# Kernel optimization log

Measured on AMD Instinct MI355X. Metric: run time of the kernel, lower is better.

Reference implementation:

```python
import jax, jax.numpy as jnp
import numpy as np

N = 50000      # num nodes
E = 1_600_000  # num edges
D = 64         # in_dim == hidden_dim
H = 4          # heads
C = 16         # head_dim = hidden_dim // heads
NEG = 0.2      # leaky_relu negative slope (PyG GATConv default)


def setup_inputs() -> dict:
    key = jax.random.key(0)
    ks = jax.random.split(key, 20)
    f = lambda k, s: (jax.random.normal(k, s, jnp.float32) * 0.1)
    return dict(
        node_features=jax.random.normal(ks[0], (N, D), jnp.float32),
        edge_index=jax.random.randint(ks[1], (2, E), 0, N, dtype=jnp.int32),
        edge_type=jax.random.randint(ks[2], (E,), 0, 5, dtype=jnp.int32),
        edge_attr=jax.random.normal(ks[3], (E, 1), jnp.float32),
        # GAT layer 1 (PyG GATConv: lin has no bias, att_* are [H,C], final bias [H*C])
        W1=f(ks[4], (D, H * C)), att_src1=f(ks[5], (H, C)), att_dst1=f(ks[6], (H, C)),
        We1=f(ks[7], (1, H * C)), att_e1=f(ks[8], (H, C)), b1=jnp.zeros((H * C,), jnp.float32),
        # GAT layer 2
        W2=f(ks[9], (D, H * C)), att_src2=f(ks[10], (H, C)), att_dst2=f(ks[11], (H, C)),
        We2=f(ks[12], (1, H * C)), att_e2=f(ks[13], (H, C)), b2=jnp.zeros((H * C,), jnp.float32),
        # LayerNorms
        g1=jnp.ones((D,), jnp.float32), beta1=jnp.zeros((D,), jnp.float32),
        g2=jnp.ones((D,), jnp.float32), beta2=jnp.zeros((D,), jnp.float32),
        # output head
        Wout=f(ks[14], (D, 1)), bout=jnp.zeros((1,), jnp.float32),
    )


def _layernorm(x, g, b, eps=1e-5):
    mu = x.mean(-1, keepdims=True)
    v = ((x - mu) ** 2).mean(-1, keepdims=True)
    return (x - mu) * jax.lax.rsqrt(v + eps) * g + b


def _seg_softmax(alpha, dst, n):
    # numerically stable segment softmax over incoming edges of each dst node
    m = jax.ops.segment_max(alpha, dst, num_segments=n)
    m = jnp.where(jnp.isfinite(m), m, 0.0)
    ex = jnp.exp(alpha - m[dst])
    den = jax.ops.segment_sum(ex, dst, num_segments=n)
    return ex / (den[dst] + 1e-16)


def _gatconv(x, src, dst, eattr, W, a_s, a_d, We, a_e, b, n):
    xs = (x @ W).reshape(n, H, C)                       # [N,H,C]
    a_src = jnp.einsum('nhc,hc->nh', xs, a_s)           # [N,H]
    a_dst = jnp.einsum('nhc,hc->nh', xs, a_d)           # [N,H]
    ee = (eattr @ We).reshape(-1, H, C)                 # [E',H,C]
    a_edge = jnp.einsum('ehc,hc->eh', ee, a_e)          # [E',H]
    alpha = a_src[src] + a_dst[dst] + a_edge            # [E',H]
    alpha = jax.nn.leaky_relu(alpha, NEG)
    alpha = _seg_softmax(alpha, dst, n)                 # [E',H]
    msg = xs[src] * alpha[..., None]                    # [E',H,C] gather-weighted messages
    out = jax.ops.segment_sum(msg, dst, num_segments=n) # scatter-aggregate
    return out.reshape(n, H * C) + b


def reference(node_features, edge_index, edge_type, edge_attr,
              W1, att_src1, att_dst1, We1, att_e1, b1,
              W2, att_src2, att_dst2, We2, att_e2, b2,
              g1, beta1, g2, beta2, Wout, bout):
    src, dst = edge_index[0], edge_index[1]
    # PyG add_self_loops(fill_value='mean'): self-loop edge_attr = mean of edge_attr over incoming edges
    cnt = jax.ops.segment_sum(jnp.ones((E,), jnp.float32), dst, num_segments=N)
    loop_attr = jax.ops.segment_sum(edge_attr, dst, num_segments=N) / jnp.maximum(cnt, 1.0)[:, None]
    loops = jnp.arange(N, dtype=src.dtype)
    src2 = jnp.concatenate([src, loops])
    dst2 = jnp.concatenate([dst, loops])
    ea = jnp.concatenate([edge_attr, loop_attr], axis=0)

    residual = node_features  # in_dim == hidden_dim -> no res_proj
    h = _gatconv(node_features, src2, dst2, ea, W1, att_src1, att_dst1, We1, att_e1, b1, N)
    h = jax.nn.elu(_layernorm(h + residual, g1, beta1))
    residual = h
    h = _gatconv(h, src2, dst2, ea, W2, att_src2, att_dst2, We2, att_e2, b2, N)
    h = jax.nn.elu(_layernorm(h + residual, g2, beta2))
    return h @ Wout + bout
```

## Files before the change

### kernel.cpp

```cpp
#include <hip/hip_runtime.h>
#include <hip/hip_bf16.h>
#include <cfloat>

#define NN 50000
#define NE 1600000
#define NEG 0.2f
#define NBKT 782
#define BNODE 64
#define P1_TILE 2048
#define P1_BLOCKS 782
#define BCAP 2560
#define SLOTS 96
#define L2E 1.4426950408889634f

typedef __attribute__((ext_vector_type(8))) short bf8_t;
typedef __attribute__((ext_vector_type(4))) float f4_t;

__device__ __forceinline__ float bf16bits_to_f(unsigned v) {
  return __uint_as_float(v << 16);
}
__device__ __forceinline__ unsigned f_to_bf16bits(float f) {
  unsigned u = __float_as_uint(f);
  return (u + 0x7fffu + ((u >> 16) & 1u)) >> 16;
}

__global__ __launch_bounds__(256) void bin_kernel(
    const int* __restrict__ src, const int* __restrict__ dst,
    const float* __restrict__ ea, int* __restrict__ gcnt,
    int2* __restrict__ gbuf) {
  __shared__ int lcnt[NBKT];
  __shared__ int lcur[NBKT];
  int t = threadIdx.x;
  for (int i = t; i < NBKT; i += 256) lcnt[i] = 0;
  __syncthreads();
  int e0 = blockIdx.x * P1_TILE;
  int bb[8], vx[8], vy[8];
#pragma unroll
  for (int k = 0; k < 8; ++k) {
    int e = e0 + k * 256 + t;
    if (e < NE) {
      int d = dst[e];
      bb[k] = d >> 6;
      vx[k] = ((d & 63) << 16) | src[e];
      vy[k] = __float_as_int(ea[e]);
      atomicAdd(&lcnt[bb[k]], 1);
    } else {
      bb[k] = -1;
    }
  }
  __syncthreads();
  for (int i = t; i < NBKT; i += 256) lcur[i] = atomicAdd(&gcnt[i], lcnt[i]);
  __syncthreads();
#pragma unroll
  for (int k = 0; k < 8; ++k) {
    if (bb[k] >= 0) {
      int pos = atomicAdd(&lcur[bb[k]], 1);
      if (pos < BCAP) gbuf[(size_t)bb[k] * BCAP + pos] = make_int2(vx[k], vy[k]);
    }
  }
}

__global__ __launch_bounds__(256) void build_kernel(
    const int* __restrict__ gcnt, const int2* __restrict__ gbuf,
    int* __restrict__ cnt, unsigned* __restrict__ csr) {
  __shared__ int lc[BNODE];
  int t = threadIdx.x;
  int b = blockIdx.x;
  if (t < BNODE) lc[t] = 0;
  __syncthreads();
  int len = gcnt[b]; if (len > BCAP) len = BCAP;
  const int2* buf = gbuf + (size_t)b * BCAP;
  for (int i = t; i < len; i += 256) {
    int2 v = buf[i];
    int dl = (v.x >> 16) & 63;
    int s = v.x & 0xffff;
    int pos = atomicAdd(&lc[dl], 1);
    if (pos < SLOTS) {
      unsigned eb = ((unsigned)v.y) & 0xffff0000u;
      csr[(size_t)(b * BNODE + dl) * SLOTS + pos] = eb | (unsigned)s;
    }
  }
  __syncthreads();
  if (t < BNODE) {
    int n = b * BNODE + t;
    if (n < NN) cnt[n] = min(lc[t], SLOTS);
  }
}

__device__ __forceinline__ bf8_t pack8(const float* p) {
  bf8_t r;
#pragma unroll
  for (int i = 0; i < 8; ++i) r[i] = (short)f_to_bf16bits(p[i]);
  return r;
}

template <bool FP32IN>
__global__ __launch_bounds__(256) void gemm_mfma_kernel(
    const void* __restrict__ xin, const float* __restrict__ W,
    const float* __restrict__ att_s, const float* __restrict__ att_d,
    unsigned short* __restrict__ xsb, float* __restrict__ a_src,
    float* __restrict__ a_dst) {
  __shared__ unsigned short Wt[64][68];
  int t = threadIdx.x;
  for (int i = t; i < 4096; i += 256) {
    int k = i >> 6, n = i & 63;
    Wt[n][k] = (unsigned short)f_to_bf16bits(W[i]);
  }
  __syncthreads();
  int lane = t & 63, wave = t >> 6;
  int quad = lane >> 4, n16 = lane & 15;

  bf8_t bfrag[4][2];
#pragma unroll
  for (int nt = 0; nt < 4; ++nt)
#pragma unroll
    for (int kk = 0; kk < 2; ++kk)
      bfrag[nt][kk] = *(const bf8_t*)&Wt[nt * 16 + n16][kk * 32 + quad * 8];

  float as4[4], ad4[4];
#pragma unroll
  for (int nt = 0; nt < 4; ++nt) {
    as4[nt] = att_s[nt * 16 + n16];
    ad4[nt] = att_d[nt * 16 + n16];
  }

  int r0w = blockIdx.x * 128 + wave * 32;
#pragma unroll
  for (int tile = 0; tile < 2; ++tile) {
    int r0 = r0w + tile * 16;
    int rowA = r0 + n16; if (rowA > NN - 1) rowA = NN - 1;
    bf8_t af0, af1;
    if (FP32IN) {
      const float* xr = (const float*)xin + (size_t)rowA * 64 + quad * 8;
      af0 = pack8(xr);
      af1 = pack8(xr + 32);
    } else {
      const bf8_t* xrow =
          (const bf8_t*)((const unsigned short*)xin + (size_t)rowA * 64);
      af0 = xrow[quad];
      af1 = xrow[4 + quad];
    }
#pragma unroll
    for (int nt = 0; nt < 4; ++nt) {
      f4_t acc = {0.f, 0.f, 0.f, 0.f};
      acc = __builtin_amdgcn_mfma_f32_16x16x32_bf16(af0, bfrag[nt][0], acc, 0, 0, 0);
      acc = __builtin_amdgcn_mfma_f32_16x16x32_bf16(af1, bfrag[nt][1], acc, 0, 0, 0);
#pragma unroll
      for (int reg = 0; reg < 4; ++reg) {
        int row = r0 + quad * 4 + reg;
        float v = acc[reg];
        if (row < NN)
          xsb[(size_t)row * 64 + nt * 16 + n16] = (unsigned short)f_to_bf16bits(v);
        float p = v * as4[nt];
        float q = v * ad4[nt];
#pragma unroll
        for (int off = 8; off; off >>= 1) {
          p += __shfl_xor(p, off, 16);
          q += __shfl_xor(q, off, 16);
        }
        if (n16 == 0 && row < NN) {
          a_src[row * 4 + nt] = p * L2E;
          a_dst[row * 4 + nt] = q * L2E;
        }
      }
    }
  }
}

template <bool HEAD>
__global__ __launch_bounds__(256) void aggregate_kernel(
    const int* __restrict__ cnt, const unsigned* __restrict__ csr,
    const unsigned short* __restrict__ xsb, const float* __restrict__ a_src,
    const float* __restrict__ a_dst, const float* __restrict__ We,
    const float* __restrict__ att_e, const float* __restrict__ bias,
    const float* __restrict__ res, const float* __restrict__ g,
    const float* __restrict__ beta, const float* __restrict__ Wout,
    const float* __restrict__ bout, float* __restrict__ out,
    unsigned short* __restrict__ out_b) {
  __shared__ __align__(16) uint2 rec[4][64][4];
  int t = threadIdx.x;
  int lane = t & 63, wave = t >> 6;
  int n = blockIdx.x * 4 + wave;
  int d2 = lane & 31;
  int hb = d2 >> 3;
  int half = lane >> 5;

  float sp = We[lane] * att_e[lane];
#pragma unroll
  for (int off = 8; off; off >>= 1) sp += __shfl_xor(sp, off, 16);
  sp *= L2E;
  float s0 = __shfl(sp, 0, 64), s1 = __shfl(sp, 16, 64);
  float s2 = __shfl(sp, 32, 64), s3 = __shfl(sp, 48, 64);

  const float4 adv = *(const float4*)(a_dst + (size_t)n * 4);

  int dn = cnt[n];
  int r0 = n * SLOTS, r1 = r0 + dn;
  float accx = 0.f, accy = 0.f, den = 0.f, easum = 0.f;
  const uint2* rpb = &rec[wave][half][hb];
  const char* xd = (const char*)xsb + d2 * 4;

  for (int base = r0; base < r1; base += 64) {
    int c = r1 - base; if (c > 64) c = 64;
    int e = base + lane;
    unsigned ce = (e < r1) ? csr[e] : 0u;
    float ea = __uint_as_float(ce & 0xffff0000u);
    easum += ea;
    unsigned soff = (ce & 0xffffu) * 128u;
    float ex0 = 0.f, ex1 = 0.f, ex2 = 0.f, ex3 = 0.f;
    if (e < r1) {
      const float4 av = *(const float4*)(a_src + (size_t)(ce & 0xffffu) * 4);
      float a0 = av.x + fmaf(ea, s0, adv.x); a0 = fmaxf(a0, NEG * a0);
      float a1 = av.y + fmaf(ea, s1, adv.y); a1 = fmaxf(a1, NEG * a1);
      float a2 = av.z + fmaf(ea, s2, adv.z); a2 = fmaxf(a2, NEG * a2);
      float a3 = av.w + fmaf(ea, s3, adv.w); a3 = fmaxf(a3, NEG * a3);
      ex0 = exp2f(a0); ex1 = exp2f(a1); ex2 = exp2f(a2); ex3 = exp2f(a3);
    }
    uint4* wp = (uint4*)&rec[wave][lane][0];
    wp[0] = make_uint4(soff, __float_as_uint(ex0), soff, __float_as_uint(ex1));
    wp[1] = make_uint4(soff, __float_as_uint(ex2), soff, __float_as_uint(ex3));
    int c8 = (c + 7) & ~7;
    for (int j = 0; j < c8; j += 8) {
      uint2 va = rpb[j * 4];
      uint2 vb = rpb[j * 4 + 8];
      uint2 vc = rpb[j * 4 + 16];
      uint2 vd = rpb[j * 4 + 24];
      unsigned ua = *(const unsigned*)(xd + va.x);
      unsigned ub = *(const unsigned*)(xd + vb.x);
      unsigned uc = *(const unsigned*)(xd + vc.x);
      unsigned ud = *(const unsigned*)(xd + vd.x);
      float efa = __uint_as_float(va.y), efb = __uint_as_float(vb.y);
      float efc = __uint_as_float(vc.y), efd = __uint_as_float(vd.y);
      den += (efa + efb) + (efc + efd);
      accx = fmaf(efa, __uint_as_float(ua << 16), accx);
      accy = fmaf(efa, __uint_as_float(ua & 0xffff0000u), accy);
      accx = fmaf(efb, __uint_as_float(ub << 16), accx);
      accy = fmaf(efb, __uint_as_float(ub & 0xffff0000u), accy);
      accx = fmaf(efc, __uint_as_float(uc << 16), accx);
      accy = fmaf(efc, __uint_as_float(uc & 0xffff0000u), accy);
      accx = fmaf(efd, __uint_as_float(ud << 16), accx);
      accy = fmaf(efd, __uint_as_float(ud & 0xffff0000u), accy);
    }
  }

  den += __shfl_xor(den, 32, 64);
  accx += __shfl_xor(accx, 32, 64);
  accy += __shfl_xor(accy, 32, 64);
#pragma unroll
  for (int off = 32; off; off >>= 1) easum += __shfl_xor(easum, off, 64);

  float loop_ea = easum / fmaxf((float)dn, 1.0f);
  float as_h = a_src[(size_t)n * 4 + hb];
  float adn = (hb == 0) ? adv.x : (hb == 1) ? adv.y : (hb == 2) ? adv.z : adv.w;
  float sph = (hb == 0) ? s0 : (hb == 1) ? s1 : (hb == 2) ? s2 : s3;
  float a_self = as_h + fmaf(loop_ea, sph, adn);
  a_self = fmaxf(a_self, NEG * a_self);
  float ex_self = exp2f(a_self);
  den += ex_self;
  unsigned un = *(const unsigned*)((const char*)xsb + (size_t)n * 128 + d2 * 4);
  accx = fmaf(ex_self, __uint_as_float(un << 16), accx);
  accy = fmaf(ex_self, __uint_as_float(un & 0xffff0000u), accy);

  float rden = 1.f / (den + 1e-16f);
  const float2 bi = *(const float2*)(bias + d2 * 2);
  const float2 rsd = *(const float2*)(res + (size_t)n * 64 + d2 * 2);
  float vx = accx * rden + bi.x + rsd.x;
  float vy = accy * rden + bi.y + rsd.y;
  float s = vx + vy;
#pragma unroll
  for (int off = 32; off; off >>= 1) s += __shfl_xor(s, off, 64);
  float mu = s * (1.0f / 128.0f);
  float dx = vx - mu, dy = vy - mu;
  float var = dx * dx + dy * dy;
#pragma unroll
  for (int off = 32; off; off >>= 1) var += __shfl_xor(var, off, 64);
  var *= (1.0f / 128.0f);
  float rstd = rsqrtf(var + 1e-5f);
  const float2 gg = *(const float2*)(g + d2 * 2);
  const float2 bb = *(const float2*)(beta + d2 * 2);
  float yx = dx * rstd * gg.x + bb.x;
  float yy = dy * rstd * gg.y + bb.y;
  yx = yx > 0.f ? yx : expm1f(yx);
  yy = yy > 0.f ? yy : expm1f(yy);
  if (HEAD) {
    const float2 wv = *(const float2*)(Wout + d2 * 2);
    float p = yx * wv.x + yy * wv.y;
#pragma unroll
    for (int off = 32; off; off >>= 1) p += __shfl_xor(p, off, 64);
    if (lane == 0) out[n] = p * 0.5f + bout[0];
  } else if (lane < 32) {
    *(float2*)(out + (size_t)n * 64 + d2 * 2) = make_float2(yx, yy);
    unsigned ob = f_to_bf16bits(yx) | (f_to_bf16bits(yy) << 16);
    *(unsigned*)(out_b + (size_t)n * 64 + d2 * 2) = ob;
  }
}

extern "C" void kernel_launch(void* const* d_in, const int* in_sizes, int n_in,
                              void* d_out, int out_size, void* d_ws,
                              size_t ws_size, hipStream_t stream) {
  const float* node_features = (const float*)d_in[0];
  const int* edge_index = (const int*)d_in[1];
  const int* src = edge_index;
  const int* dst = edge_index + NE;
  const float* edge_attr = (const float*)d_in[3];
  const float* W1 = (const float*)d_in[4];
  const float* att_src1 = (const float*)d_in[5];
  const float* att_dst1 = (const float*)d_in[6];
  const float* We1 = (const float*)d_in[7];
  const float* att_e1 = (const float*)d_in[8];
  const float* b1 = (const float*)d_in[9];
  const float* W2 = (const float*)d_in[10];
  const float* att_src2 = (const float*)d_in[11];
  const float* att_dst2 = (const float*)d_in[12];
  const float* We2 = (const float*)d_in[13];
  const float* att_e2 = (const float*)d_in[14];
  const float* b2 = (const float*)d_in[15];
  const float* g1 = (const float*)d_in[16];
  const float* beta1 = (const float*)d_in[17];
  const float* g2 = (const float*)d_in[18];
  const float* beta2 = (const float*)d_in[19];
  const float* Wout = (const float*)d_in[20];
  const float* bout = (const float*)d_in[21];
  float* out = (float*)d_out;

  char* ws = (char*)d_ws;
  size_t o = 0;
  auto alloc = [&](size_t bytes) {
    void* p = ws + o;
    o += (bytes + 255) & ~(size_t)255;
    return p;
  };
  int* gcnt = (int*)alloc((size_t)NBKT * 4);
  int2* gbuf = (int2*)alloc((size_t)NBKT * BCAP * 8);
  int* cnt = (int*)alloc((size_t)NN * 4);
  unsigned* csr = (unsigned*)alloc((size_t)NN * SLOTS * 4);
  unsigned short* xsb = (unsigned short*)alloc((size_t)NN * 64 * 2);
  unsigned short* h1b = (unsigned short*)alloc((size_t)NN * 64 * 2);
  float* a_srcb = (float*)alloc((size_t)NN * 4 * 4);
  float* a_dstb = (float*)alloc((size_t)NN * 4 * 4);
  float* h1 = (float*)alloc((size_t)NN * 64 * 4);

  hipMemsetAsync(gcnt, 0, (size_t)NBKT * 4, stream);

  bin_kernel<<<P1_BLOCKS, 256, 0, stream>>>(src, dst, edge_attr, gcnt, gbuf);
  build_kernel<<<NBKT, 256, 0, stream>>>(gcnt, gbuf, cnt, csr);

  gemm_mfma_kernel<true><<<391, 256, 0, stream>>>(
      node_features, W1, att_src1, att_dst1, xsb, a_srcb, a_dstb);
  aggregate_kernel<false><<<NN / 4, 256, 0, stream>>>(
      cnt, csr, xsb, a_srcb, a_dstb, We1, att_e1, b1, node_features, g1, beta1,
      nullptr, nullptr, h1, h1b);

  gemm_mfma_kernel<false><<<391, 256, 0, stream>>>(
      h1b, W2, att_src2, att_dst2, xsb, a_srcb, a_dstb);
  aggregate_kernel<true><<<NN / 4, 256, 0, stream>>>(
      cnt, csr, xsb, a_srcb, a_dstb, We2, att_e2, b2, h1, g2, beta2, Wout, bout,
      out, nullptr);
}
```

Measured before the change: 270.2 us.

## Fold attention vectors into extended GEMM weights and halve bucket size

Adds a prep kernel that precomputes W·att_src and W·att_dst, scales them by log2(e), and appends them as 8 extra bf16 columns to a packed weight matrix. The GEMM then computes attention logits with a fifth MFMA tile instead of using shuffle reductions. The GEMM block now covers 64 rows and the grid is doubled. Edge binning uses 32-node buckets with half the capacity, giving twice as many build blocks. The trade-offs are that the logits are now computed from bf16-rounded fused weights, which changes precision, and that the smaller buckets raise the chance of overflowing BCAP.

Result: no change. 266.6 us (-1.4%).

```diff
diff --git a/kernel.cpp b/kernel.cpp
--- a/kernel.cpp
+++ b/kernel.cpp
@@ -5,11 +5,11 @@
 #define NN 50000
 #define NE 1600000
 #define NEG 0.2f
-#define NBKT 782
-#define BNODE 64
+#define NBKT 1563
+#define BNODE 32
 #define P1_TILE 2048
 #define P1_BLOCKS 782
-#define BCAP 2560
+#define BCAP 1280
 #define SLOTS 96
 #define L2E 1.4426950408889634f
 
@@ -22,6 +22,38 @@
 __device__ __forceinline__ unsigned f_to_bf16bits(float f) {
   unsigned u = __float_as_uint(f);
   return (u + 0x7fffu + ((u >> 16) & 1u)) >> 16;
+}
+
+__global__ __launch_bounds__(256) void prep_kernel(
+    const float* __restrict__ W1, const float* __restrict__ as1,
+    const float* __restrict__ ad1, unsigned short* __restrict__ We1,
+    const float* __restrict__ W2, const float* __restrict__ as2,
+    const float* __restrict__ ad2, unsigned short* __restrict__ We2) {
+  const float* W = blockIdx.x ? W2 : W1;
+  const float* as = blockIdx.x ? as2 : as1;
+  const float* ad = blockIdx.x ? ad2 : ad1;
+  unsigned short* Wx = blockIdx.x ? We2 : We1;
+  int t = threadIdx.x;
+  if (t < 64) {
+    const float* wr = W + t * 64;
+#pragma unroll
+    for (int h = 0; h < 4; ++h) {
+      float ps = 0.f, pd = 0.f;
+#pragma unroll
+      for (int c = 0; c < 16; ++c) {
+        ps = fmaf(wr[h * 16 + c], as[h * 16 + c], ps);
+        pd = fmaf(wr[h * 16 + c], ad[h * 16 + c], pd);
+      }
+      Wx[t * 80 + 64 + h] = (unsigned short)f_to_bf16bits(ps * L2E);
+      Wx[t * 80 + 68 + h] = (unsigned short)f_to_bf16bits(pd * L2E);
+    }
+#pragma unroll
+    for (int j = 72; j < 80; ++j) Wx[t * 80 + j] = 0;
+  }
+  for (int i = t; i < 4096; i += 256) {
+    int k = i >> 6, n = i & 63;
+    Wx[k * 80 + n] = (unsigned short)f_to_bf16bits(W[i]);
+  }
 }
 
 __global__ __launch_bounds__(256) void bin_kernel(
@@ -40,8 +72,8 @@
     int e = e0 + k * 256 + t;
     if (e < NE) {
       int d = dst[e];
-      bb[k] = d >> 6;
-      vx[k] = ((d & 63) << 16) | src[e];
+      bb[k] = d >> 5;
+      vx[k] = ((d & 31) << 16) | src[e];
       vy[k] = __float_as_int(ea[e]);
       atomicAdd(&lcnt[bb[k]], 1);
     } else {
@@ -72,7 +104,7 @@
   const int2* buf = gbuf + (size_t)b * BCAP;
   for (int i = t; i < len; i += 256) {
     int2 v = buf[i];
-    int dl = (v.x >> 16) & 63;
+    int dl = (v.x >> 16) & 31;
     int s = v.x & 0xffff;
     int pos = atomicAdd(&lc[dl], 1);
     if (pos < SLOTS) {
@@ -96,71 +128,59 @@
 
 template <bool FP32IN>
 __global__ __launch_bounds__(256) void gemm_mfma_kernel(
-    const void* __restrict__ xin, const float* __restrict__ W,
-    const float* __restrict__ att_s, const float* __restrict__ att_d,
+    const void* __restrict__ xin, const unsigned short* __restrict__ Wext,
     unsigned short* __restrict__ xsb, float* __restrict__ a_src,
     float* __restrict__ a_dst) {
-  __shared__ unsigned short Wt[64][68];
-  int t = threadIdx.x;
-  for (int i = t; i < 4096; i += 256) {
-    int k = i >> 6, n = i & 63;
-    Wt[n][k] = (unsigned short)f_to_bf16bits(W[i]);
+  __shared__ unsigned short Wt[80][68];
+  int t = threadIdx.x;
+  for (int i = t; i < 5120; i += 256) {
+    int k = i / 80, n = i - k * 80;
+    Wt[n][k] = Wext[i];
   }
   __syncthreads();
   int lane = t & 63, wave = t >> 6;
   int quad = lane >> 4, n16 = lane & 15;
 
-  bf8_t bfrag[4][2];
-#pragma unroll
-  for (int nt = 0; nt < 4; ++nt)
+  bf8_t bfrag[5][2];
+#pragma unroll
+  for (int nt = 0; nt < 5; ++nt)
 #pragma unroll
     for (int kk = 0; kk < 2; ++kk)
       bfrag[nt][kk] = *(const bf8_t*)&Wt[nt * 16 + n16][kk * 32 + quad * 8];
 
-  float as4[4], ad4[4];
-#pragma unroll
-  for (int nt = 0; nt < 4; ++nt) {
-    as4[nt] = att_s[nt * 16 + n16];
-    ad4[nt] = att_d[nt * 16 + n16];
-  }
-
-  int r0w = blockIdx.x * 128 + wave * 32;
-#pragma unroll
-  for (int tile = 0; tile < 2; ++tile) {
-    int r0 = r0w + tile * 16;
-    int rowA = r0 + n16; if (rowA > NN - 1) rowA = NN - 1;
-    bf8_t af0, af1;
-    if (FP32IN) {
-      const float* xr = (const float*)xin + (size_t)rowA * 64 + quad * 8;
-      af0 = pack8(xr);
-      af1 = pack8(xr + 32);
-    } else {
-      const bf8_t* xrow =
-          (const bf8_t*)((const unsigned short*)xin + (size_t)rowA * 64);
-      af0 = xrow[quad];
-      af1 = xrow[4 + quad];
-    }
-#pragma unroll
-    for (int nt = 0; nt < 4; ++nt) {
-      f4_t acc = {0.f, 0.f, 0.f, 0.f};
-      acc = __builtin_amdgcn_mfma_f32_16x16x32_bf16(af0, bfrag[nt][0], acc, 0, 0, 0);
-      acc = __builtin_amdgcn_mfma_f32_16x16x32_bf16(af1, bfrag[nt][1], acc, 0, 0, 0);
+  int r0 = blockIdx.x * 64 + wave * 16;
+  int rowA = r0 + n16; if (rowA > NN - 1) rowA = NN - 1;
+  bf8_t af0, af1;
+  if (FP32IN) {
+    const float* xr = (const float*)xin + (size_t)rowA * 64 + quad * 8;
+    af0 = pack8(xr);
+    af1 = pack8(xr + 32);
+  } else {
+    const bf8_t* xrow =
+        (const bf8_t*)((const unsigned short*)xin + (size_t)rowA * 64);
+    af0 = xrow[quad];
+    af1 = xrow[4 + quad];
+  }
+#pragma unroll
+  for (int nt = 0; nt < 5; ++nt) {
+    f4_t acc = {0.f, 0.f, 0.f, 0.f};
+    acc = __builtin_amdgcn_mfma_f32_16x16x32_bf16(af0, bfrag[nt][0], acc, 0, 0, 0);
+    acc = __builtin_amdgcn_mfma_f32_16x16x32_bf16(af1, bfrag[nt][1], acc, 0, 0, 0);
+    if (nt < 4) {
 #pragma unroll
       for (int reg = 0; reg < 4; ++reg) {
         int row = r0 + quad * 4 + reg;
-        float v = acc[reg];
         if (row < NN)
-          xsb[(size_t)row * 64 + nt * 16 + n16] = (unsigned short)f_to_bf16bits(v);
-        float p = v * as4[nt];
-        float q = v * ad4[nt];
-#pragma unroll
-        for (int off = 8; off; off >>= 1) {
-          p += __shfl_xor(p, off, 16);
-          q += __shfl_xor(q, off, 16);
-        }
-        if (n16 == 0 && row < NN) {
-          a_src[row * 4 + nt] = p * L2E;
-          a_dst[row * 4 + nt] = q * L2E;
+          xsb[(size_t)row * 64 + nt * 16 + n16] =
+              (unsigned short)f_to_bf16bits(acc[reg]);
+      }
+    } else {
+#pragma unroll
+      for (int reg = 0; reg < 4; ++reg) {
+        int row = r0 + quad * 4 + reg;
+        if (row < NN && n16 < 8) {
+          if (n16 < 4) a_src[row * 4 + n16] = acc[reg];
+          else a_dst[row * 4 + (n16 - 4)] = acc[reg];
         }
       }
     }
@@ -336,23 +356,28 @@
   unsigned* csr = (unsigned*)alloc((size_t)NN * SLOTS * 4);
   unsigned short* xsb = (unsigned short*)alloc((size_t)NN * 64 * 2);
   unsigned short* h1b = (unsigned short*)alloc((size_t)NN * 64 * 2);
+  unsigned short* Wext1 = (unsigned short*)alloc(64 * 80 * 2);
+  unsigned short* Wext2 = (unsigned short*)alloc(64 * 80 * 2);
   float* a_srcb = (float*)alloc((size_t)NN * 4 * 4);
   float* a_dstb = (float*)alloc((size_t)NN * 4 * 4);
   float* h1 = (float*)alloc((size_t)NN * 64 * 4);
 
   hipMemsetAsync(gcnt, 0, (size_t)NBKT * 4, stream);
 
+  prep_kernel<<<2, 256, 0, stream>>>(W1, att_src1, att_dst1, Wext1, W2,
+                                     att_src2, att_dst2, Wext2);
+
   bin_kernel<<<P1_BLOCKS, 256, 0, stream>>>(src, dst, edge_attr, gcnt, gbuf);
   build_kernel<<<NBKT, 256, 0, stream>>>(gcnt, gbuf, cnt, csr);
 
-  gemm_mfma_kernel<true><<<391, 256, 0, stream>>>(
-      node_features, W1, att_src1, att_dst1, xsb, a_srcb, a_dstb);
+  gemm_mfma_kernel<true><<<782, 256, 0, stream>>>(node_features, Wext1, xsb,
+                                                  a_srcb, a_dstb);
   aggregate_kernel<false><<<NN / 4, 256, 0, stream>>>(
       cnt, csr, xsb, a_srcb, a_dstb, We1, att_e1, b1, node_features, g1, beta1,
       nullptr, nullptr, h1, h1b);
 
-  gemm_mfma_kernel<false><<<391, 256, 0, stream>>>(
-      h1b, W2, att_src2, att_dst2, xsb, a_srcb, a_dstb);
+  gemm_mfma_kernel<false><<<782, 256, 0, stream>>>(h1b, Wext2, xsb, a_srcb,
+                                                   a_dstb);
   aggregate_kernel<true><<<NN / 4, 256, 0, stream>>>(
       cnt, csr, xsb, a_srcb, a_dstb, We2, att_e2, b2, h1, g2, beta2, Wout, bout,
       out, nullptr);
```
